# Performance work log

Hardware: AMD Instinct MI355X
Metric: run time of the kernel (lower is better)

## Reference

```python
import jax, jax.numpy as jnp
import numpy as np

N = 100000
E = 1600000
C = 64          # hidden_channels
F_IN = 3
F_OUT = 3
N_MP = 2        # message-passing layers


def _lin(k, fan_in, fan_out):
    kw, kb = jax.random.split(k)
    bound = 1.0 / np.sqrt(fan_in)
    W = jax.random.uniform(kw, (fan_in, fan_out), jnp.float32, -bound, bound)
    b = jax.random.uniform(kb, (fan_out,), jnp.float32, -bound, bound)
    return W, b


def setup_inputs() -> dict:
    key = jax.random.key(0)
    ks = jax.random.split(key, 32)
    x = jax.random.normal(ks[0], (N, F_IN), jnp.float32)
    pos = jax.random.normal(ks[1], (N, 3), jnp.float32)
    edge_index = jax.random.randint(ks[2], (2, E), 0, N, jnp.int64)

    enc_W0, enc_b0 = _lin(ks[3], F_IN, C)
    enc_W1, enc_b1 = _lin(ks[4], C, C)
    dec_W0, dec_b0 = _lin(ks[5], C, C)
    dec_W1, dec_b1 = _lin(ks[6], C, F_OUT)

    # stacked params for the N_MP message-passing layers
    eW0, eb0, eW1, eb1 = [], [], [], []
    nW0, nb0, nW1, nb1 = [], [], [], []
    for i in range(N_MP):
        W, b = _lin(ks[7 + 4 * i], 3 * C + 3, C); eW0.append(W); eb0.append(b)
        W, b = _lin(ks[8 + 4 * i], C, C);         eW1.append(W); eb1.append(b)
        W, b = _lin(ks[9 + 4 * i], 2 * C, C);     nW0.append(W); nb0.append(b)
        W, b = _lin(ks[10 + 4 * i], C, C);        nW1.append(W); nb1.append(b)
    stack = lambda xs: jnp.stack(xs, axis=0)
    return {
        "x": x, "pos": pos, "edge_index": edge_index,
        "enc_W0": enc_W0, "enc_b0": enc_b0, "enc_W1": enc_W1, "enc_b1": enc_b1,
        "dec_W0": dec_W0, "dec_b0": dec_b0, "dec_W1": dec_W1, "dec_b1": dec_b1,
        "mp_eW0": stack(eW0), "mp_eb0": stack(eb0),
        "mp_eW1": stack(eW1), "mp_eb1": stack(eb1),
        "mp_nW0": stack(nW0), "mp_nb0": stack(nb0),
        "mp_nW1": stack(nW1), "mp_nb1": stack(nb1),
    }


def reference(x, pos, edge_index,
              enc_W0, enc_b0, enc_W1, enc_b1,
              dec_W0, dec_b0, dec_W1, dec_b1,
              mp_eW0, mp_eb0, mp_eW1, mp_eb1,
              mp_nW0, mp_nb0, mp_nW1, mp_nb1):
    act = jax.nn.elu
    src, dst = edge_index[0], edge_index[1]

    # node encoder (2-layer MLP, activation between layers only)
    h = act(x @ enc_W0 + enc_b0)
    h = h @ enc_W1 + enc_b1

    pos_diff = pos[src] - pos[dst]  # [E, 3], constant across MP layers

    for i in range(N_MP):
        x_nei = h[src]               # [E, C]
        x_own = h[dst]               # [E, C]
        ea = jnp.concatenate([x_nei, x_own, x_nei - x_own, pos_diff], axis=1)
        ea = act(ea @ mp_eW0[i] + mp_eb0[i])
        ea = ea @ mp_eW1[i] + mp_eb1[i]
        # EdgeAggregation(aggr='add'): scatter-add edge features to target nodes
        agg = jax.ops.segment_sum(ea, dst, num_segments=N)  # [N, C]
        u = jnp.concatenate([h, agg], axis=1)                # [N, 2C]
        u = act(u @ mp_nW0[i] + mp_nb0[i])
        u = u @ mp_nW1[i] + mp_nb1[i]
        h = h + u  # residual

    # node decoder
    out = act(h @ dec_W0 + dec_b0)
    out = out @ dec_W1 + dec_b1
    return out
```

## Files before the change

kernel.cpp:

```cpp
#include <hip/hip_runtime.h>
#include <hip/hip_bf16.h>

#define NN 100000
#define NE 1600000
#define NBKT 391
#define BCAP 4608

typedef __hip_bfloat16 bf16;
typedef unsigned short u16;
typedef unsigned int u32;
typedef short bshort8 __attribute__((ext_vector_type(8)));
typedef float f32x4 __attribute__((ext_vector_type(4)));
typedef float f32x2 __attribute__((ext_vector_type(2)));
typedef int int4u __attribute__((ext_vector_type(4), aligned(4)));
typedef unsigned int uint2u __attribute__((ext_vector_type(2), aligned(8)));

__device__ __forceinline__ float b2f_raw(u16 u) {
    unsigned int w = ((unsigned int)u) << 16;
    float f; __builtin_memcpy(&f, &w, 4); return f;
}
__device__ __forceinline__ float uplo(u32 u) {
    u32 w = u << 16; float f; __builtin_memcpy(&f, &w, 4); return f;
}
__device__ __forceinline__ float uphi(u32 u) {
    u32 w = u & 0xFFFF0000u; float f; __builtin_memcpy(&f, &w, 4); return f;
}
__device__ __forceinline__ u16 f2bu(float f) {
    bf16 h = __float2bfloat16(f); u16 u; __builtin_memcpy(&u, &h, 2); return u;
}
__device__ __forceinline__ float eluf(float x) { return x > 0.f ? x : __expf(x) - 1.f; }
__device__ __forceinline__ int4 ld4_nt(const int* p) {
    int4u v = __builtin_nontemporal_load((const int4u*)p);
    return make_int4(v.x, v.y, v.z, v.w);
}
__device__ __forceinline__ uint2 ld2_nt(const u32* p) {
    uint2u v = __builtin_nontemporal_load((const uint2u*)p);
    return make_uint2(v.x, v.y);
}
__device__ __forceinline__ void st2_nt(u32* p, u32 a, u32 b) {
    uint2u v; v.x = a; v.y = b;
    __builtin_nontemporal_store(v, (uint2u*)p);
}

#define LOG2E 1.4426950408889634f
#define LN2F  0.6931471805599453f

#define OFF_ENC_W0 0
#define OFF_ENC_B0 192
#define OFF_ENC_W1 256
#define OFF_ENC_B1 4352
#define OFF_DEC_W0 4416
#define OFF_DEC_B0 8512
#define OFF_DEC_W1 8576
#define OFF_DEC_B1 8768
#define OFF_EW0    8832
#define OFF_EB0    33792
#define OFF_EW1    33920
#define OFF_EB1    42112
#define OFF_NW0    42240
#define OFF_NB0    58624
#define OFF_NW1    58752
#define OFF_NB1    66944
#define OFF_WF     67072
#define OFF_BFOLD  75264
#define WBLK_WORDS 75392

#define SWZ_V   12288
#define SWZ_N0  24576
#define SWZ_N1  45056
#define SWZ_DC  53248
#define SWZ_ENC 57344
#define SWZ_U16 61440

__global__ void probe_kernel(const u16* __restrict__ xr,
                             const unsigned int* __restrict__ er,
                             int* __restrict__ flags, int* __restrict__ gcursor) {
    int tid = threadIdx.x;
    gcursor[tid] = 0;
    if (tid >= 64) return;
    int lane = tid;
    int wild = 0, oddnz = 0;
#pragma unroll
    for (int k = 0; k < 4; ++k) {
        int e = (xr[lane + k * 64] >> 7) & 0xFF;
        if (e > 140 || (e < 90 && e != 0)) wild++;
    }
#pragma unroll
    for (int k = 0; k < 2; ++k)
        if (er[1 + 2 * (lane + k * 64)] != 0u) oddnz++;
#pragma unroll
    for (int off = 32; off; off >>= 1) {
        wild += __shfl_down(wild, off);
        oddnz += __shfl_down(oddnz, off);
    }
    if (lane == 0) { flags[0] = (wild > 16) ? 1 : 0; flags[1] = (oddnz < 8) ? 1 : 0; }
}

struct WPtrs { const void* p[16]; };

__global__ void canon_weights(WPtrs wp, float* __restrict__ wblk,
                              const int* __restrict__ flags) {
    const int offs[16] = {OFF_ENC_W0, OFF_ENC_B0, OFF_ENC_W1, OFF_ENC_B1,
                          OFF_DEC_W0, OFF_DEC_B0, OFF_DEC_W1, OFF_DEC_B1,
                          OFF_EW0, OFF_EB0, OFF_EW1, OFF_EB1,
                          OFF_NW0, OFF_NB0, OFF_NW1, OFF_NB1};
    const int ns[16]   = {192, 64, 4096, 64, 4096, 64, 192, 3,
                          24960, 128, 8192, 128, 16384, 128, 8192, 128};
    int t = blockIdx.y;
    int i = blockIdx.x * blockDim.x + threadIdx.x;
    if (i >= ns[t]) return;
    const void* s = wp.p[t];
    float v = flags[0] ? ((const float*)s)[i] : b2f_raw(((const u16*)s)[i]);
    wblk[offs[t] + i] = v;
}

__global__ void prep_wf(float* __restrict__ wblk) {
    int idx = blockIdx.x * 256 + threadIdx.x;
    if (idx < 8192) {
        int l = idx >> 12, r = idx & 4095, k = r >> 6, c = r & 63;
        const float* e1 = wblk + OFF_EW1 + l * 4096 + k * 64;
        const float* n0 = wblk + OFF_NW0 + l * 8192 + 64 * 64;
        float s = 0.f;
#pragma unroll 8
        for (int m = 0; m < 64; ++m) s += e1[m] * n0[m * 64 + c];
        wblk[OFF_WF + idx] = s;
    } else if (idx < 8320) {
        int i2 = idx - 8192;
        int l = i2 >> 6, c = i2 & 63;
        const float* b1 = wblk + OFF_EB1 + l * 64;
        const float* n0 = wblk + OFF_NW0 + l * 8192 + 64 * 64;
        float s = 0.f;
#pragma unroll 8
        for (int m = 0; m < 64; ++m) s += b1[m] * n0[m * 64 + c];
        wblk[OFF_BFOLD + i2] = s;
    }
}

__global__ void prep_swz(const float* __restrict__ wblk, u16* __restrict__ swz) {
    int t = blockIdx.x * 256 + threadIdx.x;
    if (t >= SWZ_U16) return;
    float v = 0.f;
    if (t < SWZ_N0) {
        int isV = (t >= SWZ_V);
        int t2 = isV ? t - SWZ_V : t;
        int l = t2 / 6144, r = t2 % 6144;
        int ks = r >> 11, nt = (r >> 9) & 3, lane = (r >> 3) & 63, j = r & 7;
        int k = ks * 32 + ((lane >> 4) & 3) * 8 + j;
        int n = nt * 16 + (lane & 15);
        const float* W = wblk + OFF_EW0 + l * 12480;
        if (k < 64)
            v = isV ? (W[(64 + k) * 64 + n] - W[(128 + k) * 64 + n])
                    : (W[k * 64 + n] + W[(128 + k) * 64 + n]);
        else if (k < 67) {
            v = W[(192 + (k - 64)) * 64 + n];
            if (isV) v = -v;
        }
    } else if (t < SWZ_N1) {
        int t2 = t - SWZ_N0;
        int l = t2 / 10240, r = t2 % 10240;
        int ks = r >> 11, nt = (r >> 9) & 3, lane = (r >> 3) & 63, j = r & 7;
        int k = ks * 32 + ((lane >> 4) & 3) * 8 + j;
        int n = nt * 16 + (lane & 15);
        if (k < 64)        v = wblk[OFF_NW0 + l * 8192 + k * 64 + n];
        else if (k < 128)  v = wblk[OFF_WF + l * 4096 + (k - 64) * 64 + n];
        else if (k == 128) v = wblk[OFF_BFOLD + l * 64 + n];
    } else if (t < SWZ_DC) {
        int t2 = t - SWZ_N1;
        int l = t2 / 4096, r = t2 % 4096;
        int ks = r >> 11, nt = (r >> 9) & 3, lane = (r >> 3) & 63, j = r & 7;
        int k = ks * 32 + ((lane >> 4) & 3) * 8 + j;
        int n = nt * 16 + (lane & 15);
        v = wblk[OFF_NW1 + l * 4096 + k * 64 + n];
    } else if (t < SWZ_ENC) {
        int r = t - SWZ_DC;
        int ks = r >> 11, nt = (r >> 9) & 3, lane = (r >> 3) & 63, j = r & 7;
        int k = ks * 32 + ((lane >> 4) & 3) * 8 + j;
        int n = nt * 16 + (lane & 15);
        v = wblk[OFF_DEC_W0 + k * 64 + n];
    } else {
        int r = t - SWZ_ENC;
        int ks = r >> 11, nt = (r >> 9) & 3, lane = (r >> 3) & 63, j = r & 7;
        int k = ks * 32 + ((lane >> 4) & 3) * 8 + j;
        int n = nt * 16 + (lane & 15);
        v = wblk[OFF_ENC_W1 + k * 64 + n];
    }
    swz[t] = f2bu(v);
}

__global__ __launch_bounds__(1024) void passA_bin(
    const void* __restrict__ eiraw, const int* __restrict__ flags,
    u32* __restrict__ epk_b, int* __restrict__ gcursor) {
    __shared__ int hist[NBKT];
    __shared__ int binstart[NBKT];
    __shared__ int gbase_l[NBKT];
    __shared__ int fill[NBKT];
    __shared__ int sc[512];
    __shared__ u32 stage[4096];
    __shared__ u16 slotbin[4096];
    int tid = threadIdx.x;
    for (int i = tid; i < NBKT; i += 1024) hist[i] = 0;
    __syncthreads();
    int base = blockIdx.x * 4096;
    int total = NE - base; if (total > 4096) total = 4096;
    bool i64 = flags[1] != 0;
    u32 ed[4]; int bn[4];
#pragma unroll
    for (int k = 0; k < 4; ++k) {
        int e = base + tid + k * 1024;
        bn[k] = -1;
        if (e < NE) {
            int s, d;
            if (i64) {
                s = (int)((const long long*)eiraw)[e];
                d = (int)((const long long*)eiraw)[(size_t)NE + e];
            } else {
                s = ((const int*)eiraw)[e];
                d = ((const int*)eiraw)[(size_t)NE + e];
            }
            if ((unsigned)s >= NN) s = 0;
            if ((unsigned)d >= NN) d = 0;
            ed[k] = (u32)s | ((u32)(d & 255) << 17);
            bn[k] = d >> 8;
            atomicAdd(&hist[bn[k]], 1);
        }
    }
    __syncthreads();
    if (tid < 512) sc[tid] = (tid < NBKT) ? hist[tid] : 0;
    __syncthreads();
    for (int d = 1; d < 512; d <<= 1) {
        int v = (tid >= d && tid < 512) ? sc[tid - d] : 0;
        __syncthreads();
        if (tid < 512) sc[tid] += v;
        __syncthreads();
    }
    if (tid < NBKT) {
        binstart[tid] = sc[tid] - hist[tid];
        fill[tid] = 0;
        gbase_l[tid] = hist[tid] ? atomicAdd(&gcursor[tid], hist[tid]) : 0;
    }
    __syncthreads();
#pragma unroll
    for (int k = 0; k < 4; ++k) {
        if (bn[k] >= 0) {
            int p = binstart[bn[k]] + atomicAdd(&fill[bn[k]], 1);
            stage[p] = ed[k];
            slotbin[p] = (u16)bn[k];
        }
    }
    __syncthreads();
    for (int i = tid; i < total; i += 1024) {
        int b = slotbin[i];
        int gp = gbase_l[b] + (i - binstart[b]);
        if (gp < BCAP) epk_b[(size_t)b * BCAP + gp] = stage[i];
    }
}

__global__ __launch_bounds__(1024) void passB_sort(
    const u32* __restrict__ epk_b, const int* __restrict__ gcursor,
    int* __restrict__ srcs, int* __restrict__ start) {
    __shared__ int gsc[512];
    __shared__ int h256[256];
    __shared__ int off256[256];
    __shared__ int sc[256];
    __shared__ u32 stage[BCAP];
    int b = blockIdx.x, tid = threadIdx.x;
    if (tid < 512) {
        int v = 0;
        if (tid < NBKT) { v = gcursor[tid]; if (v > BCAP) v = BCAP; }
        gsc[tid] = v;
    }
    for (int i = tid; i < 256; i += 1024) h256[i] = 0;
    __syncthreads();
    for (int d = 1; d < 512; d <<= 1) {
        int u = (tid >= d && tid < 512) ? gsc[tid - d] : 0;
        __syncthreads();
        if (tid < 512) gsc[tid] += u;
        __syncthreads();
    }
    int cnt = gcursor[b]; if (cnt > BCAP) cnt = BCAP;
    int gb = gsc[b] - cnt;
    u32 ed[5]; int dl[5];
#pragma unroll
    for (int k = 0; k < 5; ++k) {
        int i = tid + k * 1024;
        dl[k] = -1;
        if (i < cnt) {
            ed[k] = epk_b[(size_t)b * BCAP + i];
            dl[k] = (int)(ed[k] >> 17);
            atomicAdd(&h256[dl[k]], 1);
        }
    }
    __syncthreads();
    if (tid < 256) sc[tid] = h256[tid];
    __syncthreads();
    for (int d = 1; d < 256; d <<= 1) {
        int v = (tid >= d && tid < 256) ? sc[tid - d] : 0;
        __syncthreads();
        if (tid < 256) sc[tid] += v;
        __syncthreads();
    }
    if (tid < 256) {
        off256[tid] = sc[tid] - h256[tid];
        start[b * 256 + tid] = gb + sc[tid] - h256[tid];
    }
    __syncthreads();
#pragma unroll
    for (int k = 0; k < 5; ++k) {
        if (dl[k] >= 0) {
            int p = atomicAdd(&off256[dl[k]], 1);
            stage[p] = ed[k];
        }
    }
    __syncthreads();
    for (int i = tid; i < cnt; i += 1024)
        srcs[gb + i] = (int)(stage[i] & 0x1FFFFu) << 5;
}

__global__ __launch_bounds__(512) void enc_uv(
    const void* __restrict__ xraw, const void* __restrict__ praw,
    const float* __restrict__ wblk, const u16* __restrict__ swzE,
    const u16* __restrict__ swzU, const u16* __restrict__ swzV,
    u16* __restrict__ hb, u16* __restrict__ pos4b,
    u16* __restrict__ U, u16* __restrict__ V,
    const int* __restrict__ flags) {
    __shared__ __attribute__((aligned(16))) u16 sE[4096];
    __shared__ __attribute__((aligned(16))) u16 sU[6144];
    __shared__ __attribute__((aligned(16))) u16 sV[6144];
    __shared__ __attribute__((aligned(16))) u16 sP[8][16 * 72];
    int tid = threadIdx.x;
    for (int i = tid; i < 512; i += 512) ((uint4*)sE)[i] = ((const uint4*)swzE)[i];
    for (int i = tid; i < 768; i += 512) {
        ((uint4*)sU)[i] = ((const uint4*)swzU)[i];
        ((uint4*)sV)[i] = ((const uint4*)swzV)[i];
    }
    __syncthreads();
    int wid = tid >> 6, lane = tid & 63;
    int m16 = lane & 15, half = lane >> 4;
    int g = blockIdx.x * 8 + wid;
    if (g >= NN / 16) return;
    int n0 = g * 16 + m16;
    bool isf = flags[0] != 0;
    float x0, x1, x2;
    if (isf) {
        x0 = ((const float*)xraw)[n0 * 3 + 0];
        x1 = ((const float*)xraw)[n0 * 3 + 1];
        x2 = ((const float*)xraw)[n0 * 3 + 2];
    } else {
        x0 = b2f_raw(((const u16*)xraw)[n0 * 3 + 0]);
        x1 = b2f_raw(((const u16*)xraw)[n0 * 3 + 1]);
        x2 = b2f_raw(((const u16*)xraw)[n0 * 3 + 2]);
    }
    u16 pk0 = 0, pk1 = 0, pk2 = 0;
    if (half == 0) {
        float p0 = isf ? ((const float*)praw)[n0 * 3 + 0] : b2f_raw(((const u16*)praw)[n0 * 3 + 0]);
        float p1 = isf ? ((const float*)praw)[n0 * 3 + 1] : b2f_raw(((const u16*)praw)[n0 * 3 + 1]);
        float p2 = isf ? ((const float*)praw)[n0 * 3 + 2] : b2f_raw(((const u16*)praw)[n0 * 3 + 2]);
        pk0 = f2bu(p0); pk1 = f2bu(p1); pk2 = f2bu(p2);
        *(ushort4*)(pos4b + (size_t)n0 * 4) = make_ushort4(pk0, pk1, pk2, 0);
    }
    const float* W0 = wblk + OFF_ENC_W0;
    const float* b0 = wblk + OFF_ENC_B0;
    bshort8 af0, af1;
#pragma unroll
    for (int j = 0; j < 8; ++j) {
        int c = half * 8 + j;
        float v = b0[c] + x0 * W0[c] + x1 * W0[64 + c] + x2 * W0[128 + c];
        af0[j] = (short)f2bu(eluf(v));
        int c2 = 32 + c;
        float v2 = b0[c2] + x0 * W0[c2] + x1 * W0[64 + c2] + x2 * W0[128 + c2];
        af1[j] = (short)f2bu(eluf(v2));
    }
    const bshort8* BE = (const bshort8*)sE;
    f32x4 acc[4];
#pragma unroll
    for (int nt = 0; nt < 4; ++nt) {
        float b = wblk[OFF_ENC_B1 + nt * 16 + m16];
        acc[nt] = f32x4{b, b, b, b};
    }
#pragma unroll
    for (int nt = 0; nt < 4; ++nt)
        acc[nt] = __builtin_amdgcn_mfma_f32_16x16x32_bf16(af0, BE[nt * 64 + lane], acc[nt], 0, 0, 0);
#pragma unroll
    for (int nt = 0; nt < 4; ++nt)
        acc[nt] = __builtin_amdgcn_mfma_f32_16x16x32_bf16(af1, BE[(4 + nt) * 64 + lane], acc[nt], 0, 0, 0);
    u16* myP = sP[wid];
#pragma unroll
    for (int nt = 0; nt < 4; ++nt)
#pragma unroll
        for (int r = 0; r < 4; ++r) {
            size_t ix = (size_t)(g * 16 + half * 4 + r) * 64 + nt * 16 + m16;
            u16 hv = f2bu(acc[nt][r]);
            hb[ix] = hv;
            myP[(half * 4 + r) * 72 + nt * 16 + m16] = hv;
        }
    bshort8 ah0 = *(const bshort8*)(myP + m16 * 72 + 0 * 32 + half * 8);
    bshort8 ah1 = *(const bshort8*)(myP + m16 * 72 + 1 * 32 + half * 8);
    bshort8 ap;
#pragma unroll
    for (int j = 0; j < 8; ++j) ap[j] = 0;
    if (half == 0) { ap[0] = (short)pk0; ap[1] = (short)pk1; ap[2] = (short)pk2; }
    const bshort8* BU = (const bshort8*)sU;
    const bshort8* BV = (const bshort8*)sV;
    const float* eb0p = wblk + OFF_EB0;
    f32x4 aU[4], aV[4];
#pragma unroll
    for (int nt = 0; nt < 4; ++nt) {
        float bv = eb0p[nt * 16 + m16];
        aU[nt] = f32x4{0.f, 0.f, 0.f, 0.f};
        aV[nt] = f32x4{bv, bv, bv, bv};
    }
#pragma unroll
    for (int nt = 0; nt < 4; ++nt) {
        aU[nt] = __builtin_amdgcn_mfma_f32_16x16x32_bf16(ah0, BU[nt * 64 + lane], aU[nt], 0, 0, 0);
        aV[nt] = __builtin_amdgcn_mfma_f32_16x16x32_bf16(ah0, BV[nt * 64 + lane], aV[nt], 0, 0, 0);
    }
#pragma unroll
    for (int nt = 0; nt < 4; ++nt) {
        aU[nt] = __builtin_amdgcn_mfma_f32_16x16x32_bf16(ah1, BU[(4 + nt) * 64 + lane], aU[nt], 0, 0, 0);
        aV[nt] = __builtin_amdgcn_mfma_f32_16x16x32_bf16(ah1, BV[(4 + nt) * 64 + lane], aV[nt], 0, 0, 0);
    }
#pragma unroll
    for (int nt = 0; nt < 4; ++nt) {
        aU[nt] = __builtin_amdgcn_mfma_f32_16x16x32_bf16(ap, BU[(8 + nt) * 64 + lane], aU[nt], 0, 0, 0);
        aV[nt] = __builtin_amdgcn_mfma_f32_16x16x32_bf16(ap, BV[(8 + nt) * 64 + lane], aV[nt], 0, 0, 0);
    }
#pragma unroll
    for (int nt = 0; nt < 4; ++nt)
#pragma unroll
        for (int r = 0; r < 4; ++r) {
            size_t ix = (size_t)(g * 16 + half * 4 + r) * 64 + nt * 16 + m16;
            U[ix] = f2bu(aU[nt][r] * LOG2E);
            V[ix] = f2bu(aV[nt][r] * LOG2E);
        }
}

__global__ __launch_bounds__(256, 4) void edge_sum(
    const u32* __restrict__ U32, const u32* __restrict__ V32,
    const int* __restrict__ srcs, const int* __restrict__ start,
    u32* __restrict__ Sb, int totalwaves) {
    int tid = threadIdx.x;
    int w = blockIdx.x * 4 + (tid >> 6);
    int lane = tid & 63;
    int eo = lane >> 4, co = lane & 15;
    u32 coff = (u32)(co << 1);
    int e0 = eo << 2;
    int nb = (int)((long long)w * NN / totalwaves);
    int ne = (int)((long long)(w + 1) * NN / totalwaves);
    if (nb >= ne) return;

    int s0 = start[nb];
    int s1 = start[nb + 1];
    int4 pfa = ld4_nt(srcs + s0 + e0);
    int4 pfb = ld4_nt(srcs + s0 + 16 + e0);
    uint2 pv = ld2_nt(V32 + (((u32)nb << 5) + coff));

    const f32x2 z2 = {0.f, 0.f}, o2 = {1.f, 1.f};

    for (int n = nb; n < ne; ++n) {
        int cnt = s1 - s0;
        int4 ca = pfa, cb = pfb;
        uint2 vv = pv;
        int s0n = s1;
        int s1n = start[n + 2];
        {
            int vn = (n + 1 < NN) ? (n + 1) : (NN - 1);
            pfa = ld4_nt(srcs + s0n + e0);
            pfb = ld4_nt(srcs + s0n + 16 + e0);
            pv = ld2_nt(V32 + (((u32)vn << 5) + coff));
        }

        f32x2 v01 = {uplo(vv.x), uphi(vv.x)};
        f32x2 v23 = {uplo(vv.y), uphi(vv.y)};
        f32x2 aA01 = z2, aA23 = z2, aB01 = z2, aB23 = z2;

        auto gat = [&](int spre) -> uint2 {
            return *(const uint2*)(U32 + ((u32)spre + coff));
        };
        auto body = [&](uint2 uu) {
            f32x2 x01 = f32x2{uplo(uu.x), uphi(uu.x)} + v01;
            f32x2 x23 = f32x2{uplo(uu.y), uphi(uu.y)} + v23;
            f32x2 e01 = {__builtin_amdgcn_exp2f(x01.x), __builtin_amdgcn_exp2f(x01.y)};
            f32x2 e23 = {__builtin_amdgcn_exp2f(x23.x), __builtin_amdgcn_exp2f(x23.y)};
            aA01 += __builtin_elementwise_max(x01, z2);
            aA23 += __builtin_elementwise_max(x23, z2);
            aB01 += __builtin_elementwise_min(e01, o2);
            aB23 += __builtin_elementwise_min(e23, o2);
        };
        auto bodym = [&](uint2 uu, bool val) {
            f32x2 x01 = f32x2{uplo(uu.x), uphi(uu.x)} + v01;
            f32x2 x23 = f32x2{uplo(uu.y), uphi(uu.y)} + v23;
            f32x2 e01 = {__builtin_amdgcn_exp2f(x01.x), __builtin_amdgcn_exp2f(x01.y)};
            f32x2 e23 = {__builtin_amdgcn_exp2f(x23.x), __builtin_amdgcn_exp2f(x23.y)};
            f32x2 mA01 = __builtin_elementwise_max(x01, z2);
            f32x2 mA23 = __builtin_elementwise_max(x23, z2);
            f32x2 mB01 = __builtin_elementwise_min(e01, o2);
            f32x2 mB23 = __builtin_elementwise_min(e23, o2);
            aA01 += val ? mA01 : z2;
            aA23 += val ? mA23 : z2;
            aB01 += val ? mB01 : z2;
            aB23 += val ? mB23 : z2;
        };

        if (cnt >= 32) {
            uint2 u0 = gat(ca.x), u1 = gat(ca.y), u2 = gat(ca.z), u3 = gat(ca.w);
            uint2 u4 = gat(cb.x), u5 = gat(cb.y), u6 = gat(cb.z), u7 = gat(cb.w);
            body(u0); body(u1); body(u2); body(u3);
            body(u4); body(u5); body(u6); body(u7);
            int g = 32;
            for (; g + 16 <= cnt; g += 16) {
                int4 cc = ld4_nt(srcs + s0 + g + e0);
                uint2 w0 = gat(cc.x), w1 = gat(cc.y), w2 = gat(cc.z), w3 = gat(cc.w);
                body(w0); body(w1); body(w2); body(w3);
            }
            if (g < cnt) {
                int4 cc = ld4_nt(srcs + s0 + g + e0);
                int r = cnt - g;
                bool m0 = (e0 < r), m1 = (e0 + 1 < r), m2 = (e0 + 2 < r), m3 = (e0 + 3 < r);
                uint2 w0 = gat(m0 ? cc.x : 0), w1 = gat(m1 ? cc.y : 0);
                uint2 w2 = gat(m2 ? cc.z : 0), w3 = gat(m3 ? cc.w : 0);
                bodym(w0, m0); bodym(w1, m1); bodym(w2, m2); bodym(w3, m3);
            }
        } else if (cnt > 16) {
            int r = cnt - 16;
            bool m0 = (e0 < r), m1 = (e0 + 1 < r), m2 = (e0 + 2 < r), m3 = (e0 + 3 < r);
            uint2 u0 = gat(ca.x), u1 = gat(ca.y), u2 = gat(ca.z), u3 = gat(ca.w);
            uint2 u4 = gat(m0 ? cb.x : 0), u5 = gat(m1 ? cb.y : 0);
            uint2 u6 = gat(m2 ? cb.z : 0), u7 = gat(m3 ? cb.w : 0);
            body(u0); body(u1); body(u2); body(u3);
            bodym(u4, m0); bodym(u5, m1); bodym(u6, m2); bodym(u7, m3);
        } else if (cnt > 0) {
            bool m0 = (e0 < cnt), m1 = (e0 + 1 < cnt), m2 = (e0 + 2 < cnt), m3 = (e0 + 3 < cnt);
            uint2 u0 = gat(m0 ? ca.x : 0), u1 = gat(m1 ? ca.y : 0);
            uint2 u2 = gat(m2 ? ca.z : 0), u3 = gat(m3 ? ca.w : 0);
            bodym(u0, m0); bodym(u1, m1); bodym(u2, m2); bodym(u3, m3);
        }

        f32x2 t01 = aA01 * LN2F + aB01;
        f32x2 t23 = aA23 * LN2F + aB23;
        float t0 = t01.x, t1 = t01.y, t2 = t23.x, t3 = t23.y;
        t0 += __shfl_xor(t0, 16); t0 += __shfl_xor(t0, 32);
        t1 += __shfl_xor(t1, 16); t1 += __shfl_xor(t1, 32);
        t2 += __shfl_xor(t2, 16); t2 += __shfl_xor(t2, 32);
        t3 += __shfl_xor(t3, 16); t3 += __shfl_xor(t3, 32);
        if (eo == 0) {
            float cf = (float)cnt;
            u32 p0 = (u32)f2bu(t0 - cf) | ((u32)f2bu(t1 - cf) << 16);
            u32 p1 = (u32)f2bu(t2 - cf) | ((u32)f2bu(t3 - cf) << 16);
            st2_nt(Sb + (((u32)n << 5) + coff), p0, p1);
        }
        s0 = s0n; s1 = s1n;
    }
}

__global__ __launch_bounds__(512) void node_uv(
    u16* __restrict__ hb, const u16* __restrict__ Sb,
    const int* __restrict__ start, const float* __restrict__ wblk,
    const u16* __restrict__ swz, const u16* __restrict__ pos4b,
    u16* __restrict__ U, u16* __restrict__ V) {
    __shared__ __attribute__((aligned(16))) u16 sN0[10240];
    __shared__ __attribute__((aligned(16))) u16 sN1[4096];
    __shared__ __attribute__((aligned(16))) u16 sU[6144];
    __shared__ __attribute__((aligned(16))) u16 sV[6144];
    __shared__ __attribute__((aligned(16))) u16 sP[8][16 * 72];
    int tid = threadIdx.x;
    {
        const uint4* s0 = (const uint4*)(swz + SWZ_N0);
        const uint4* s1 = (const uint4*)(swz + SWZ_N1);
        const uint4* su = (const uint4*)(swz + 6144);
        const uint4* sv = (const uint4*)(swz + SWZ_V + 6144);
        for (int i = tid; i < 1280; i += 512) ((uint4*)sN0)[i] = s0[i];
        for (int i = tid; i < 512; i += 512)  ((uint4*)sN1)[i] = s1[i];
        for (int i = tid; i < 768; i += 512) {
            ((uint4*)sU)[i] = su[i];
            ((uint4*)sV)[i] = sv[i];
        }
    }
    __syncthreads();
    int wid = tid >> 6, lane = tid & 63;
    int m16 = lane & 15, half = lane >> 4;
    int g = blockIdx.x * 8 + wid;
    if (g >= NN / 16) return;
    int n0 = g * 16 + m16;
    const float* b0 = wblk + OFF_NB0;
    const float* b1 = wblk + OFF_NB1;
    const bshort8* B0 = (const bshort8*)sN0;
    const bshort8* B1 = (const bshort8*)sN1;
    u16* myP = sP[wid];

    bshort8 afh0 = *(const bshort8*)(hb + (size_t)n0 * 64 + half * 8);
    bshort8 afh1 = *(const bshort8*)(hb + (size_t)n0 * 64 + 32 + half * 8);
    bshort8 afs0 = *(const bshort8*)(Sb + (size_t)n0 * 64 + half * 8);
    bshort8 afs1 = *(const bshort8*)(Sb + (size_t)n0 * 64 + 32 + half * 8);
    bshort8 afd;
#pragma unroll
    for (int j = 0; j < 8; ++j) afd[j] = 0;
    if (half == 0) {
        float deg = (float)(start[n0 + 1] - start[n0]);
        afd[0] = (short)f2bu(deg);
    }
    f32x4 acc[4];
#pragma unroll
    for (int nt = 0; nt < 4; ++nt) {
        float b = b0[nt * 16 + m16];
        acc[nt] = f32x4{b, b, b, b};
    }
#pragma unroll
    for (int nt = 0; nt < 4; ++nt)
        acc[nt] = __builtin_amdgcn_mfma_f32_16x16x32_bf16(afh0, B0[nt * 64 + lane], acc[nt], 0, 0, 0);
#pragma unroll
    for (int nt = 0; nt < 4; ++nt)
        acc[nt] = __builtin_amdgcn_mfma_f32_16x16x32_bf16(afh1, B0[(4 + nt) * 64 + lane], acc[nt], 0, 0, 0);
#pragma unroll
    for (int nt = 0; nt < 4; ++nt)
        acc[nt] = __builtin_amdgcn_mfma_f32_16x16x32_bf16(afs0, B0[(8 + nt) * 64 + lane], acc[nt], 0, 0, 0);
#pragma unroll
    for (int nt = 0; nt < 4; ++nt)
        acc[nt] = __builtin_amdgcn_mfma_f32_16x16x32_bf16(afs1, B0[(12 + nt) * 64 + lane], acc[nt], 0, 0, 0);
#pragma unroll
    for (int nt = 0; nt < 4; ++nt)
        acc[nt] = __builtin_amdgcn_mfma_f32_16x16x32_bf16(afd, B0[(16 + nt) * 64 + lane], acc[nt], 0, 0, 0);
#pragma unroll
    for (int nt = 0; nt < 4; ++nt)
#pragma unroll
        for (int r = 0; r < 4; ++r) {
            float v = acc[nt][r];
            v = eluf(v);
            myP[(half * 4 + r) * 72 + nt * 16 + m16] = f2bu(v);
        }
    f32x4 acc2[4];
#pragma unroll
    for (int nt = 0; nt < 4; ++nt) {
        float b = b1[nt * 16 + m16];
        acc2[nt] = f32x4{b, b, b, b};
    }
#pragma unroll
    for (int ks = 0; ks < 2; ++ks) {
        bshort8 av = *(const bshort8*)(myP + m16 * 72 + ks * 32 + half * 8);
#pragma unroll
        for (int nt = 0; nt < 4; ++nt)
            acc2[nt] = __builtin_amdgcn_mfma_f32_16x16x32_bf16(
                av, B1[(ks * 4 + nt) * 64 + lane], acc2[nt], 0, 0, 0);
    }
#pragma unroll
    for (int nt = 0; nt < 4; ++nt)
#pragma unroll
        for (int r = 0; r < 4; ++r) {
            size_t ix = (size_t)(g * 16 + half * 4 + r) * 64 + nt * 16 + m16;
            float v = b2f_raw(hb[ix]) + acc2[nt][r];
            u16 hv = f2bu(v);
            hb[ix] = hv;
            myP[(half * 4 + r) * 72 + nt * 16 + m16] = hv;
        }
    bshort8 ah0 = *(const bshort8*)(myP + m16 * 72 + 0 * 32 + half * 8);
    bshort8 ah1 = *(const bshort8*)(myP + m16 * 72 + 1 * 32 + half * 8);
    bshort8 ap;
#pragma unroll
    for (int j = 0; j < 8; ++j) ap[j] = 0;
    if (half == 0) {
        ushort4 pp = *(const ushort4*)(pos4b + (size_t)n0 * 4);
        ap[0] = (short)pp.x; ap[1] = (short)pp.y; ap[2] = (short)pp.z;
    }
    const bshort8* BU = (const bshort8*)sU;
    const bshort8* BV = (const bshort8*)sV;
    const float* eb0p = wblk + OFF_EB0 + 64;
    f32x4 aU[4], aV[4];
#pragma unroll
    for (int nt = 0; nt < 4; ++nt) {
        float bv = eb0p[nt * 16 + m16];
        aU[nt] = f32x4{0.f, 0.f, 0.f, 0.f};
        aV[nt] = f32x4{bv, bv, bv, bv};
    }
#pragma unroll
    for (int nt = 0; nt < 4; ++nt) {
        aU[nt] = __builtin_amdgcn_mfma_f32_16x16x32_bf16(ah0, BU[nt * 64 + lane], aU[nt], 0, 0, 0);
        aV[nt] = __builtin_amdgcn_mfma_f32_16x16x32_bf16(ah0, BV[nt * 64 + lane], aV[nt], 0, 0, 0);
    }
#pragma unroll
    for (int nt = 0; nt < 4; ++nt) {
        aU[nt] = __builtin_amdgcn_mfma_f32_16x16x32_bf16(ah1, BU[(4 + nt) * 64 + lane], aU[nt], 0, 0, 0);
        aV[nt] = __builtin_amdgcn_mfma_f32_16x16x32_bf16(ah1, BV[(4 + nt) * 64 + lane], aV[nt], 0, 0, 0);
    }
#pragma unroll
    for (int nt = 0; nt < 4; ++nt) {
        aU[nt] = __builtin_amdgcn_mfma_f32_16x16x32_bf16(ap, BU[(8 + nt) * 64 + lane], aU[nt], 0, 0, 0);
        aV[nt] = __builtin_amdgcn_mfma_f32_16x16x32_bf16(ap, BV[(8 + nt) * 64 + lane], aV[nt], 0, 0, 0);
    }
#pragma unroll
    for (int nt = 0; nt < 4; ++nt)
#pragma unroll
        for (int r = 0; r < 4; ++r) {
            size_t ix = (size_t)(g * 16 + half * 4 + r) * 64 + nt * 16 + m16;
            U[ix] = f2bu(aU[nt][r] * LOG2E);
            V[ix] = f2bu(aV[nt][r] * LOG2E);
        }
}

__global__ __launch_bounds__(512) void node_dec(
    const u16* __restrict__ hb, const u16* __restrict__ Sb,
    const int* __restrict__ start, const float* __restrict__ wblk,
    const u16* __restrict__ swz,
    void* __restrict__ out, const int* __restrict__ flags) {
    __shared__ __attribute__((aligned(16))) u16 sN0[10240];
    __shared__ __attribute__((aligned(16))) u16 sN1[4096];
    __shared__ __attribute__((aligned(16))) u16 sDec[4096];
    __shared__ __attribute__((aligned(16))) float sT[8][1048];
    int tid = threadIdx.x;
    {
        const uint4* s0 = (const uint4*)(swz + SWZ_N0 + 10240);
        const uint4* s1 = (const uint4*)(swz + SWZ_N1 + 4096);
        const uint4* sd = (const uint4*)(swz + SWZ_DC);
        for (int i = tid; i < 1280; i += 512) ((uint4*)sN0)[i] = s0[i];
        for (int i = tid; i < 512; i += 512)  ((uint4*)sN1)[i] = s1[i];
        for (int i = tid; i < 512; i += 512)  ((uint4*)sDec)[i] = sd[i];
    }
    __syncthreads();
    int wid = tid >> 6, lane = tid & 63;
    int m16 = lane & 15, half = lane >> 4;
    int g = blockIdx.x * 8 + wid;
    if (g >= NN / 16) return;
    int n0 = g * 16 + m16;
    const float* b0 = wblk + OFF_NB0 + 64;
    const float* b1 = wblk + OFF_NB1 + 64;
    const bshort8* B0 = (const bshort8*)sN0;
    const bshort8* B1 = (const bshort8*)sN1;
    const bshort8* BD = (const bshort8*)sDec;
    u16* myP = (u16*)sT[wid];
    float* sD = sT[wid];

    bshort8 afh0 = *(const bshort8*)(hb + (size_t)n0 * 64 + half * 8);
    bshort8 afh1 = *(const bshort8*)(hb + (size_t)n0 * 64 + 32 + half * 8);
    bshort8 afs0 = *(const bshort8*)(Sb + (size_t)n0 * 64 + half * 8);
    bshort8 afs1 = *(const bshort8*)(Sb + (size_t)n0 * 64 + 32 + half * 8);
    bshort8 afd;
#pragma unroll
    for (int j = 0; j < 8; ++j) afd[j] = 0;
    if (half == 0) {
        float deg = (float)(start[n0 + 1] - start[n0]);
        afd[0] = (short)f2bu(deg);
    }
    f32x4 acc[4];
#pragma unroll
    for (int nt = 0; nt < 4; ++nt) {
        float b = b0[nt * 16 + m16];
        acc[nt] = f32x4{b, b, b, b};
    }
#pragma unroll
    for (int nt = 0; nt < 4; ++nt)
        acc[nt] = __builtin_amdgcn_mfma_f32_16x16x32_bf16(afh0, B0[nt * 64 + lane], acc[nt], 0, 0, 0);
#pragma unroll
    for (int nt = 0; nt < 4; ++nt)
        acc[nt] = __builtin_amdgcn_mfma_f32_16x16x32_bf16(afh1, B0[(4 + nt) * 64 + lane], acc[nt], 0, 0, 0);
#pragma unroll
    for (int nt = 0; nt < 4; ++nt)
        acc[nt] = __builtin_amdgcn_mfma_f32_16x16x32_bf16(afs0, B0[(8 + nt) * 64 + lane], acc[nt], 0, 0, 0);
#pragma unroll
    for (int nt = 0; nt < 4; ++nt)
        acc[nt] = __builtin_amdgcn_mfma_f32_16x16x32_bf16(afs1, B0[(12 + nt) * 64 + lane], acc[nt], 0, 0, 0);
#pragma unroll
    for (int nt = 0; nt < 4; ++nt)
        acc[nt] = __builtin_amdgcn_mfma_f32_16x16x32_bf16(afd, B0[(16 + nt) * 64 + lane], acc[nt], 0, 0, 0);
#pragma unroll
    for (int nt = 0; nt < 4; ++nt)
#pragma unroll
        for (int r = 0; r < 4; ++r) {
            float v = acc[nt][r];
            v = eluf(v);
            myP[(half * 4 + r) * 72 + nt * 16 + m16] = f2bu(v);
        }
    f32x4 acc2[4];
#pragma unroll
    for (int nt = 0; nt < 4; ++nt) {
        float b = b1[nt * 16 + m16];
        acc2[nt] = f32x4{b, b, b, b};
    }
#pragma unroll
    for (int ks = 0; ks < 2; ++ks) {
        bshort8 av = *(const bshort8*)(myP + m16 * 72 + ks * 32 + half * 8);
#pragma unroll
        for (int nt = 0; nt < 4; ++nt)
            acc2[nt] = __builtin_amdgcn_mfma_f32_16x16x32_bf16(
                av, B1[(ks * 4 + nt) * 64 + lane], acc2[nt], 0, 0, 0);
    }
    float nh[4][4];
#pragma unroll
    for (int nt = 0; nt < 4; ++nt)
#pragma unroll
        for (int r = 0; r < 4; ++r) {
            size_t ix = (size_t)(g * 16 + half * 4 + r) * 64 + nt * 16 + m16;
            nh[nt][r] = b2f_raw(hb[ix]) + acc2[nt][r];
        }
#pragma unroll
    for (int nt = 0; nt < 4; ++nt)
#pragma unroll
        for (int r = 0; r < 4; ++r)
            myP[(half * 4 + r) * 72 + nt * 16 + m16] = f2bu(nh[nt][r]);
    const float* db0 = wblk + OFF_DEC_B0;
    f32x4 acc3[4];
#pragma unroll
    for (int nt = 0; nt < 4; ++nt) {
        float b = db0[nt * 16 + m16];
        acc3[nt] = f32x4{b, b, b, b};
    }
#pragma unroll
    for (int ks = 0; ks < 2; ++ks) {
        bshort8 av = *(const bshort8*)(myP + m16 * 72 + ks * 32 + half * 8);
#pragma unroll
        for (int nt = 0; nt < 4; ++nt)
            acc3[nt] = __builtin_amdgcn_mfma_f32_16x16x32_bf16(
                av, BD[(ks * 4 + nt) * 64 + lane], acc3[nt], 0, 0, 0);
    }
#pragma unroll
    for (int nt = 0; nt < 4; ++nt)
#pragma unroll
        for (int r = 0; r < 4; ++r) {
            float v = acc3[nt][r];
            v = eluf(v);
            sD[(half * 4 + r) * 65 + nt * 16 + m16] = v;
        }
    if (lane < 48) {
        int j = lane / 3, o = lane - j * 3;
        const float* dW1 = wblk + OFF_DEC_W1;
        float oacc = wblk[OFF_DEC_B1 + o];
#pragma unroll
        for (int k = 0; k < 64; ++k) oacc += sD[j * 65 + k] * dW1[k * 3 + o];
        int nn = g * 16 + j;
        if (flags[0]) ((float*)out)[nn * 3 + o] = oacc;
        else          ((bf16*)out)[nn * 3 + o] = __float2bfloat16(oacc);
    }
}

extern "C" void kernel_launch(void* const* d_in, const int* in_sizes, int n_in,
                              void* d_out, int out_size, void* d_ws, size_t ws_size,
                              hipStream_t stream) {
    int*   flags   = (int*)d_ws;
    float* wblk    = (float*)d_ws + 16;
    u16*   swz     = (u16*)(wblk + WBLK_WORDS);
    u16*   pos4b   = swz + SWZ_U16;
    int*   gcursor = (int*)(pos4b + 400000);
    int*   gbase2  = gcursor + 512;
    int*   start   = gbase2 + 512;
    int*   srcs    = start + NN + 512;
    u16*   Sb      = (u16*)(srcs + NE);
    u16*   hb      = Sb + (size_t)NN * 64;
    u16*   U       = hb + (size_t)NN * 64;
    u16*   V       = U + (size_t)NN * 64;
    u32*   epk_b   = (u32*)Sb;

    probe_kernel<<<1, 512, 0, stream>>>((const u16*)d_in[0],
                                        (const unsigned int*)d_in[2], flags, gcursor);

    WPtrs wp;
    wp.p[0] = d_in[3];  wp.p[1] = d_in[4];  wp.p[2] = d_in[5];  wp.p[3] = d_in[6];
    wp.p[4] = d_in[7];  wp.p[5] = d_in[8];  wp.p[6] = d_in[9];  wp.p[7] = d_in[10];
    wp.p[8] = d_in[11]; wp.p[9] = d_in[12]; wp.p[10] = d_in[13]; wp.p[11] = d_in[14];
    wp.p[12] = d_in[15]; wp.p[13] = d_in[16]; wp.p[14] = d_in[17]; wp.p[15] = d_in[18];
    canon_weights<<<dim3(98, 16), 256, 0, stream>>>(wp, wblk, flags);
    prep_wf<<<33, 256, 0, stream>>>(wblk);
    prep_swz<<<240, 256, 0, stream>>>(wblk, swz);

    passA_bin<<<(NE + 4095) / 4096, 1024, 0, stream>>>(d_in[2], flags, epk_b, gcursor);
    passB_sort<<<NBKT, 1024, 0, stream>>>(epk_b, gcursor, srcs, start);

    const int NODE_BLOCKS = (NN / 16 + 7) / 8;
    const int EDGE_BLOCKS = 2048;
    const int TOTALWAVES = EDGE_BLOCKS * 4;

    enc_uv<<<NODE_BLOCKS, 512, 0, stream>>>(
        d_in[0], d_in[1], wblk, swz + SWZ_ENC,
        swz, swz + SWZ_V, hb, pos4b, U, V, flags);

    edge_sum<<<EDGE_BLOCKS, 256, 0, stream>>>(
        (const u32*)U, (const u32*)V, srcs, start, (u32*)Sb, TOTALWAVES);
    node_uv<<<NODE_BLOCKS, 512, 0, stream>>>(
        hb, Sb, start, wblk, swz, pos4b, U, V);

    edge_sum<<<EDGE_BLOCKS, 256, 0, stream>>>(
        (const u32*)U, (const u32*)V, srcs, start, (u32*)Sb, TOTALWAVES);
    node_dec<<<NODE_BLOCKS, 512, 0, stream>>>(
        hb, Sb, start, wblk, swz, d_out, flags);
}
```

Measured before the change: 308.9 us.

## Split U/V/S into channel-slab layout and partition edge gather by channel slab

U, V and the aggregate S are stored as 8 channel slabs of [N][8] bf16 instead of row-major [N][64]. Each edge_sum block now handles one slab, so the gathered working set per slab (N×16 bytes) fits better in cache. Each lane fetches 4 bytes per edge and covers 16 edges per pass. The cost is 8× more re-reads of srcs/start, smaller per-lane gathers, and a longer shuffle reduction. Nontemporal loads are dropped and occupancy hints are raised.

```diff
diff --git a/kernel.cpp b/kernel.cpp
--- a/kernel.cpp
+++ b/kernel.cpp
@@ -12,8 +12,6 @@
 typedef short bshort8 __attribute__((ext_vector_type(8)));
 typedef float f32x4 __attribute__((ext_vector_type(4)));
 typedef float f32x2 __attribute__((ext_vector_type(2)));
-typedef int int4u __attribute__((ext_vector_type(4), aligned(4)));
-typedef unsigned int uint2u __attribute__((ext_vector_type(2), aligned(8)));
 
 __device__ __forceinline__ float b2f_raw(u16 u) {
     unsigned int w = ((unsigned int)u) << 16;
@@ -29,18 +27,6 @@
     bf16 h = __float2bfloat16(f); u16 u; __builtin_memcpy(&u, &h, 2); return u;
 }
 __device__ __forceinline__ float eluf(float x) { return x > 0.f ? x : __expf(x) - 1.f; }
-__device__ __forceinline__ int4 ld4_nt(const int* p) {
-    int4u v = __builtin_nontemporal_load((const int4u*)p);
-    return make_int4(v.x, v.y, v.z, v.w);
-}
-__device__ __forceinline__ uint2 ld2_nt(const u32* p) {
-    uint2u v = __builtin_nontemporal_load((const uint2u*)p);
-    return make_uint2(v.x, v.y);
-}
-__device__ __forceinline__ void st2_nt(u32* p, u32 a, u32 b) {
-    uint2u v; v.x = a; v.y = b;
-    __builtin_nontemporal_store(v, (uint2u*)p);
-}
 
 #define LOG2E 1.4426950408889634f
 #define LN2F  0.6931471805599453f
@@ -313,8 +299,9 @@
     }
     __syncthreads();
     for (int i = tid; i < cnt; i += 1024)
-        srcs[gb + i] = (int)(stage[i] & 0x1FFFFu) << 5;
-}
+        srcs[gb + i] = (int)(stage[i] & 0x1FFFFu) << 2;
+}
+
 
 __global__ __launch_bounds__(512) void enc_uv(
     const void* __restrict__ xraw, const void* __restrict__ praw,
@@ -428,125 +415,103 @@
     for (int nt = 0; nt < 4; ++nt)
 #pragma unroll
         for (int r = 0; r < 4; ++r) {
-            size_t ix = (size_t)(g * 16 + half * 4 + r) * 64 + nt * 16 + m16;
+            int node = g * 16 + half * 4 + r;
+            int c = nt * 16 + m16;
+            size_t ix = ((size_t)(c >> 3) * NN + node) * 8 + (c & 7);
             U[ix] = f2bu(aU[nt][r] * LOG2E);
             V[ix] = f2bu(aV[nt][r] * LOG2E);
         }
 }
 
-__global__ __launch_bounds__(256, 4) void edge_sum(
+__global__ __launch_bounds__(256, 8) void edge_sum(
     const u32* __restrict__ U32, const u32* __restrict__ V32,
     const int* __restrict__ srcs, const int* __restrict__ start,
-    u32* __restrict__ Sb, int totalwaves) {
+    u32* __restrict__ Sb, int totalranges) {
     int tid = threadIdx.x;
-    int w = blockIdx.x * 4 + (tid >> 6);
+    int b = blockIdx.x;
+    int s = b & 7;
+    int w = (b >> 3) * 4 + (tid >> 6);
     int lane = tid & 63;
-    int eo = lane >> 4, co = lane & 15;
-    u32 coff = (u32)(co << 1);
-    int e0 = eo << 2;
-    int nb = (int)((long long)w * NN / totalwaves);
-    int ne = (int)((long long)(w + 1) * NN / totalwaves);
+    int eo = lane >> 2, co = lane & 3;
+    const u32* Ub = U32 + (size_t)s * NN * 4;
+    const u32* Vb = V32 + (size_t)s * NN * 4;
+    u32* Sbb = Sb + (size_t)s * NN * 4;
+    int nb = (int)((long long)w * NN / totalranges);
+    int ne = (int)((long long)(w + 1) * NN / totalranges);
     if (nb >= ne) return;
 
     int s0 = start[nb];
     int s1 = start[nb + 1];
-    int4 pfa = ld4_nt(srcs + s0 + e0);
-    int4 pfb = ld4_nt(srcs + s0 + 16 + e0);
-    uint2 pv = ld2_nt(V32 + (((u32)nb << 5) + coff));
+    int pf0 = srcs[s0 + eo];
+    int pf1 = srcs[s0 + 16 + eo];
+    u32 pvw = Vb[(u32)nb * 4 + (u32)co];
 
     const f32x2 z2 = {0.f, 0.f}, o2 = {1.f, 1.f};
 
     for (int n = nb; n < ne; ++n) {
         int cnt = s1 - s0;
-        int4 ca = pfa, cb = pfb;
-        uint2 vv = pv;
+        int c0 = pf0, c1 = pf1;
+        u32 vw = pvw;
         int s0n = s1;
         int s1n = start[n + 2];
         {
             int vn = (n + 1 < NN) ? (n + 1) : (NN - 1);
-            pfa = ld4_nt(srcs + s0n + e0);
-            pfb = ld4_nt(srcs + s0n + 16 + e0);
-            pv = ld2_nt(V32 + (((u32)vn << 5) + coff));
-        }
-
-        f32x2 v01 = {uplo(vv.x), uphi(vv.x)};
-        f32x2 v23 = {uplo(vv.y), uphi(vv.y)};
-        f32x2 aA01 = z2, aA23 = z2, aB01 = z2, aB23 = z2;
-
-        auto gat = [&](int spre) -> uint2 {
-            return *(const uint2*)(U32 + ((u32)spre + coff));
+            pf0 = srcs[s0n + eo];
+            pf1 = srcs[s0n + 16 + eo];
+            pvw = Vb[(u32)vn * 4 + (u32)co];
+        }
+
+        f32x2 v01 = {uplo(vw), uphi(vw)};
+        f32x2 aA = z2, aB = z2;
+
+        auto gat = [&](u32 spre) -> u32 { return Ub[spre + (u32)co]; };
+        auto body = [&](u32 uw) {
+            f32x2 x = f32x2{uplo(uw), uphi(uw)} + v01;
+            f32x2 e = {__builtin_amdgcn_exp2f(x.x), __builtin_amdgcn_exp2f(x.y)};
+            aA += __builtin_elementwise_max(x, z2);
+            aB += __builtin_elementwise_min(e, o2);
         };
-        auto body = [&](uint2 uu) {
-            f32x2 x01 = f32x2{uplo(uu.x), uphi(uu.x)} + v01;
-            f32x2 x23 = f32x2{uplo(uu.y), uphi(uu.y)} + v23;
-            f32x2 e01 = {__builtin_amdgcn_exp2f(x01.x), __builtin_amdgcn_exp2f(x01.y)};
-            f32x2 e23 = {__builtin_amdgcn_exp2f(x23.x), __builtin_amdgcn_exp2f(x23.y)};
-            aA01 += __builtin_elementwise_max(x01, z2);
-            aA23 += __builtin_elementwise_max(x23, z2);
-            aB01 += __builtin_elementwise_min(e01, o2);
-            aB23 += __builtin_elementwise_min(e23, o2);
+        auto bodym = [&](u32 uw, bool val) {
+            f32x2 x = f32x2{uplo(uw), uphi(uw)} + v01;
+            f32x2 e = {__builtin_amdgcn_exp2f(x.x), __builtin_amdgcn_exp2f(x.y)};
+            f32x2 mA = __builtin_elementwise_max(x, z2);
+            f32x2 mB = __builtin_elementwise_min(e, o2);
+            aA += val ? mA : z2;
+            aB += val ? mB : z2;
         };
-        auto bodym = [&](uint2 uu, bool val) {
-            f32x2 x01 = f32x2{uplo(uu.x), uphi(uu.x)} + v01;
-            f32x2 x23 = f32x2{uplo(uu.y), uphi(uu.y)} + v23;
-            f32x2 e01 = {__builtin_amdgcn_exp2f(x01.x), __builtin_amdgcn_exp2f(x01.y)};
-            f32x2 e23 = {__builtin_amdgcn_exp2f(x23.x), __builtin_amdgcn_exp2f(x23.y)};
-            f32x2 mA01 = __builtin_elementwise_max(x01, z2);
-            f32x2 mA23 = __builtin_elementwise_max(x23, z2);
-            f32x2 mB01 = __builtin_elementwise_min(e01, o2);
-            f32x2 mB23 = __builtin_elementwise_min(e23, o2);
-            aA01 += val ? mA01 : z2;
-            aA23 += val ? mA23 : z2;
-            aB01 += val ? mB01 : z2;
-            aB23 += val ? mB23 : z2;
-        };
 
         if (cnt >= 32) {
-            uint2 u0 = gat(ca.x), u1 = gat(ca.y), u2 = gat(ca.z), u3 = gat(ca.w);
-            uint2 u4 = gat(cb.x), u5 = gat(cb.y), u6 = gat(cb.z), u7 = gat(cb.w);
-            body(u0); body(u1); body(u2); body(u3);
-            body(u4); body(u5); body(u6); body(u7);
+            u32 u0 = gat((u32)c0), u1 = gat((u32)c1);
+            body(u0); body(u1);
             int g = 32;
             for (; g + 16 <= cnt; g += 16) {
-                int4 cc = ld4_nt(srcs + s0 + g + e0);
-                uint2 w0 = gat(cc.x), w1 = gat(cc.y), w2 = gat(cc.z), w3 = gat(cc.w);
-                body(w0); body(w1); body(w2); body(w3);
+                int a = srcs[s0 + g + eo];
+                body(gat((u32)a));
             }
             if (g < cnt) {
-                int4 cc = ld4_nt(srcs + s0 + g + e0);
-                int r = cnt - g;
-                bool m0 = (e0 < r), m1 = (e0 + 1 < r), m2 = (e0 + 2 < r), m3 = (e0 + 3 < r);
-                uint2 w0 = gat(m0 ? cc.x : 0), w1 = gat(m1 ? cc.y : 0);
-                uint2 w2 = gat(m2 ? cc.z : 0), w3 = gat(m3 ? cc.w : 0);
-                bodym(w0, m0); bodym(w1, m1); bodym(w2, m2); bodym(w3, m3);
+                int a = srcs[s0 + g + eo];
+                bool m = eo < (cnt - g);
+                bodym(gat(m ? (u32)a : 0u), m);
             }
         } else if (cnt > 16) {
-            int r = cnt - 16;
-            bool m0 = (e0 < r), m1 = (e0 + 1 < r), m2 = (e0 + 2 < r), m3 = (e0 + 3 < r);
-            uint2 u0 = gat(ca.x), u1 = gat(ca.y), u2 = gat(ca.z), u3 = gat(ca.w);
-            uint2 u4 = gat(m0 ? cb.x : 0), u5 = gat(m1 ? cb.y : 0);
-            uint2 u6 = gat(m2 ? cb.z : 0), u7 = gat(m3 ? cb.w : 0);
-            body(u0); body(u1); body(u2); body(u3);
-            bodym(u4, m0); bodym(u5, m1); bodym(u6, m2); bodym(u7, m3);
+            bool m = eo < (cnt - 16);
+            u32 u0 = gat((u32)c0);
+            u32 u1 = gat(m ? (u32)c1 : 0u);
+            body(u0); bodym(u1, m);
         } else if (cnt > 0) {
-            bool m0 = (e0 < cnt), m1 = (e0 + 1 < cnt), m2 = (e0 + 2 < cnt), m3 = (e0 + 3 < cnt);
-            uint2 u0 = gat(m0 ? ca.x : 0), u1 = gat(m1 ? ca.y : 0);
-            uint2 u2 = gat(m2 ? ca.z : 0), u3 = gat(m3 ? ca.w : 0);
-            bodym(u0, m0); bodym(u1, m1); bodym(u2, m2); bodym(u3, m3);
-        }
-
-        f32x2 t01 = aA01 * LN2F + aB01;
-        f32x2 t23 = aA23 * LN2F + aB23;
-        float t0 = t01.x, t1 = t01.y, t2 = t23.x, t3 = t23.y;
-        t0 += __shfl_xor(t0, 16); t0 += __shfl_xor(t0, 32);
-        t1 += __shfl_xor(t1, 16); t1 += __shfl_xor(t1, 32);
-        t2 += __shfl_xor(t2, 16); t2 += __shfl_xor(t2, 32);
-        t3 += __shfl_xor(t3, 16); t3 += __shfl_xor(t3, 32);
+            bool m = eo < cnt;
+            bodym(gat(m ? (u32)c0 : 0u), m);
+        }
+
+        f32x2 t = aA * LN2F + aB;
+        float t0 = t.x, t1 = t.y;
+        t0 += __shfl_xor(t0, 4);  t1 += __shfl_xor(t1, 4);
+        t0 += __shfl_xor(t0, 8);  t1 += __shfl_xor(t1, 8);
+        t0 += __shfl_xor(t0, 16); t1 += __shfl_xor(t1, 16);
+        t0 += __shfl_xor(t0, 32); t1 += __shfl_xor(t1, 32);
         if (eo == 0) {
             float cf = (float)cnt;
-            u32 p0 = (u32)f2bu(t0 - cf) | ((u32)f2bu(t1 - cf) << 16);
-            u32 p1 = (u32)f2bu(t2 - cf) | ((u32)f2bu(t3 - cf) << 16);
-            st2_nt(Sb + (((u32)n << 5) + coff), p0, p1);
+            Sbb[(u32)n * 4 + (u32)co] = (u32)f2bu(t0 - cf) | ((u32)f2bu(t1 - cf) << 16);
         }
         s0 = s0n; s1 = s1n;
     }
@@ -589,8 +554,8 @@
 
     bshort8 afh0 = *(const bshort8*)(hb + (size_t)n0 * 64 + half * 8);
     bshort8 afh1 = *(const bshort8*)(hb + (size_t)n0 * 64 + 32 + half * 8);
-    bshort8 afs0 = *(const bshort8*)(Sb + (size_t)n0 * 64 + half * 8);
-    bshort8 afs1 = *(const bshort8*)(Sb + (size_t)n0 * 64 + 32 + half * 8);
+    bshort8 afs0 = *(const bshort8*)(Sb + ((size_t)half * NN + n0) * 8);
+    bshort8 afs1 = *(const bshort8*)(Sb + ((size_t)(4 + half) * NN + n0) * 8);
     bshort8 afd;
 #pragma unroll
     for (int j = 0; j < 8; ++j) afd[j] = 0;
@@ -689,7 +654,9 @@
     for (int nt = 0; nt < 4; ++nt)
 #pragma unroll
         for (int r = 0; r < 4; ++r) {
-            size_t ix = (size_t)(g * 16 + half * 4 + r) * 64 + nt * 16 + m16;
+            int node = g * 16 + half * 4 + r;
+            int c = nt * 16 + m16;
+            size_t ix = ((size_t)(c >> 3) * NN + node) * 8 + (c & 7);
             U[ix] = f2bu(aU[nt][r] * LOG2E);
             V[ix] = f2bu(aV[nt][r] * LOG2E);
         }
@@ -729,8 +696,8 @@
 
     bshort8 afh0 = *(const bshort8*)(hb + (size_t)n0 * 64 + half * 8);
     bshort8 afh1 = *(const bshort8*)(hb + (size_t)n0 * 64 + 32 + half * 8);
-    bshort8 afs0 = *(const bshort8*)(Sb + (size_t)n0 * 64 + half * 8);
-    bshort8 afs1 = *(const bshort8*)(Sb + (size_t)n0 * 64 + 32 + half * 8);
+    bshort8 afs0 = *(const bshort8*)(Sb + ((size_t)half * NN + n0) * 8);
+    bshort8 afs1 = *(const bshort8*)(Sb + ((size_t)(4 + half) * NN + n0) * 8);
     bshort8 afd;
 #pragma unroll
     for (int j = 0; j < 8; ++j) afd[j] = 0;
@@ -863,19 +830,19 @@
 
     const int NODE_BLOCKS = (NN / 16 + 7) / 8;
     const int EDGE_BLOCKS = 2048;
-    const int TOTALWAVES = EDGE_BLOCKS * 4;
+    const int TOTALRANGES = (EDGE_BLOCKS / 8) * 4;
 
     enc_uv<<<NODE_BLOCKS, 512, 0, stream>>>(
         d_in[0], d_in[1], wblk, swz + SWZ_ENC,
         swz, swz + SWZ_V, hb, pos4b, U, V, flags);
 
     edge_sum<<<EDGE_BLOCKS, 256, 0, stream>>>(
-        (const u32*)U, (const u32*)V, srcs, start, (u32*)Sb, TOTALWAVES);
+        (const u32*)U, (const u32*)V, srcs, start, (u32*)Sb, TOTALRANGES);
     node_uv<<<NODE_BLOCKS, 512, 0, stream>>>(
         hb, Sb, start, wblk, swz, pos4b, U, V);
 
     edge_sum<<<EDGE_BLOCKS, 256, 0, stream>>>(
-        (const u32*)U, (const u32*)V, srcs, start, (u32*)Sb, TOTALWAVES);
+        (const u32*)U, (const u32*)V, srcs, start, (u32*)Sb, TOTALRANGES);
     node_dec<<<NODE_BLOCKS, 512, 0, stream>>>(
         hb, Sb, start, wblk, swz, d_out, flags);
 }
```

Result: slower. 425.7 us (+37.8%).
